# Kernel optimization log

Hardware: AMD Instinct MI355X
Metric: run time of the kernel (lower is better)

The kernel has to match this reference:

```python
import jax, jax.numpy as jnp
import numpy as np

L = 2048         # new tokens (prefill)
HID = 4096
NH = 32          # attention heads
NKV = 8          # kv heads
HD = HID // NH   # 128
MAX = 4096       # kv-cache capacity
EPS = 1e-5


def _rope_tables(L, HD):
    inv_freq = 1.0 / (10000.0 ** (np.arange(0, HD, 2, dtype=np.float32) / HD))
    ang = np.arange(L, dtype=np.float32)[:, None] * inv_freq[None, :]  # [L, HD/2]
    ang = np.concatenate([ang, ang], axis=-1)                          # HF duplicated layout
    return jnp.asarray(np.cos(ang)), jnp.asarray(np.sin(ang))


def setup_inputs() -> dict:
    key = jax.random.key(0)
    ks = jax.random.split(key, 6)
    cos, sin = _rope_tables(L, HD)
    s = 0.02
    return {
        "x": jax.random.normal(ks[0], (L, HID), jnp.float32),
        "cos": cos,
        "sin": sin,
        "position_ids": jnp.arange(L, dtype=jnp.int64),
        "seq_len": L,
        "k_cache": jnp.zeros((MAX, NKV, HD), jnp.float32),
        "v_cache": jnp.zeros((MAX, NKV, HD), jnp.float32),
        "ln_w": jnp.ones((HID,), jnp.float32),
        "Wq": jax.random.normal(ks[1], (NH * HD, HID), jnp.float32) * s,
        "Wk": jax.random.normal(ks[2], (NKV * HD, HID), jnp.float32) * s,
        "Wv": jax.random.normal(ks[3], (NKV * HD, HID), jnp.float32) * s,
        "Wo": jax.random.normal(ks[4], (HID, NH * HD), jnp.float32) * s,
    }


def _rms_norm(x, w, eps=EPS):
    xf = x.astype(jnp.float32)
    var = jnp.mean(xf * xf, axis=-1, keepdims=True)
    return (w * (xf * jax.lax.rsqrt(var + eps))).astype(x.dtype)


def _rotate_half(x):
    x1, x2 = jnp.split(x, 2, axis=-1)
    return jnp.concatenate([-x2, x1], axis=-1)


def reference(x, cos, sin, position_ids, seq_len, k_cache, v_cache, ln_w, Wq, Wk, Wv, Wo):
    Lq, hid = x.shape
    nkv, hd = k_cache.shape[1], k_cache.shape[2]
    nh = Wq.shape[0] // hd
    g = nh // nkv

    residual = x
    h = _rms_norm(x, ln_w)

    q = (h @ Wq.T).reshape(Lq, nh, hd)
    k = (h @ Wk.T).reshape(Lq, nkv, hd)
    v = (h @ Wv.T).reshape(Lq, nkv, hd)

    # RoPE, cos/sin broadcast over heads (unsqueeze_dim=1)
    c = cos[:, None, :]
    s = sin[:, None, :]
    q = q * c + _rotate_half(q) * s
    k = k * c + _rotate_half(k) * s

    # KV-cache scatter write
    k_cache = k_cache.at[position_ids].set(k)
    v_cache = v_cache.at[position_ids].set(v)

    # prefill path (num_new_tokens > 1): causal GQA SDPA over new keys only
    scale = 1.0 / jnp.sqrt(jnp.asarray(hd, jnp.float32))
    qg = q.reshape(Lq, nkv, g, hd)
    scores = jnp.einsum('qhgd,khd->hgqk', qg, k) * scale  # [nkv, g, Lq, Lq]
    idx = jnp.arange(Lq)
    causal = idx[None, :] <= idx[:, None]                  # [Lq, Lq]
    scores = jnp.where(causal[None, None], scores, -jnp.inf)
    p = jax.nn.softmax(scores, axis=-1)
    attn = jnp.einsum('hgqk,khd->qhgd', p, v).reshape(Lq, nh * hd)

    out = residual + attn @ Wo.T
    return out, k_cache, v_cache
```

## Files before the change

### kernel.cpp

```cpp
#include <hip/hip_runtime.h>
#include <hip/hip_bf16.h>
#include <cstdint>

#define L_SEQ 2048
#define HID   4096
#define NH    32
#define NKV   8
#define HD    128
#define MAXP  4096
#define QKVD  6144
#define K_OFF 4096
#define V_OFF 5120

using bf16_t = __hip_bfloat16;
typedef __bf16 bf16x8 __attribute__((ext_vector_type(8)));
typedef float  f32x4  __attribute__((ext_vector_type(4)));
typedef short  short4v __attribute__((ext_vector_type(4)));
typedef short  short8v __attribute__((ext_vector_type(8)));

__device__ __forceinline__ void async_copy16(void* lds, const void* g) {
  __builtin_amdgcn_global_load_lds(
      (__attribute__((address_space(1))) void*)g,
      (__attribute__((address_space(3))) void*)lds, 16, 0, 0);
}

__device__ __forceinline__ f32x4 MFMA16(bf16x8 a, bf16x8 b, f32x4 c) {
  return __builtin_amdgcn_mfma_f32_16x16x32_bf16(a, b, c, 0, 0, 0);
}

__global__ __launch_bounds__(256) void rmsnorm_kernel(
    const float* __restrict__ x, const float* __restrict__ w,
    bf16_t* __restrict__ h) {
  int row = blockIdx.x, t = threadIdx.x;
  const float4* xv = (const float4*)(x + (size_t)row * HID);
  float4 v[4];
  float ss = 0.f;
#pragma unroll
  for (int i = 0; i < 4; i++) {
    v[i] = xv[i * 256 + t];
    ss += v[i].x * v[i].x + v[i].y * v[i].y + v[i].z * v[i].z + v[i].w * v[i].w;
  }
#pragma unroll
  for (int off = 32; off >= 1; off >>= 1) ss += __shfl_xor(ss, off, 64);
  __shared__ float red[4];
  if ((t & 63) == 0) red[t >> 6] = ss;
  __syncthreads();
  float rr = rsqrtf((red[0] + red[1] + red[2] + red[3]) * (1.0f / HID) + 1e-5f);
  const float4* wv = (const float4*)w;
  bf16_t* hr = h + (size_t)row * HID;
#pragma unroll
  for (int i = 0; i < 4; i++) {
    float4 wl = wv[i * 256 + t];
    bf16_t tmp[4];
    tmp[0] = __float2bfloat16(v[i].x * rr * wl.x);
    tmp[1] = __float2bfloat16(v[i].y * rr * wl.y);
    tmp[2] = __float2bfloat16(v[i].z * rr * wl.z);
    tmp[3] = __float2bfloat16(v[i].w * rr * wl.w);
    *(short4v*)(hr + (size_t)(i * 256 + t) * 4) = *(short4v*)tmp;
  }
}

__global__ __launch_bounds__(256) void cvt_bf16_kernel(
    const float* __restrict__ src, bf16_t* __restrict__ dst) {
  size_t i = ((size_t)blockIdx.x * 256 + threadIdx.x) * 8;
  float4 a = *(const float4*)(src + i);
  float4 b = *(const float4*)(src + i + 4);
  bf16_t tmp[8] = {__float2bfloat16(a.x), __float2bfloat16(a.y),
                   __float2bfloat16(a.z), __float2bfloat16(a.w),
                   __float2bfloat16(b.x), __float2bfloat16(b.y),
                   __float2bfloat16(b.z), __float2bfloat16(b.w)};
  *(short8v*)(dst + i) = *(short8v*)tmp;
}

#define STR2_(x) #x
#define STR_(x) STR2_(x)

template <int OUT_MODE>
__global__ __launch_bounds__(512, 2) void gemm256_kernel(
    const bf16_t* __restrict__ A, const bf16_t* __restrict__ B,
    bf16_t* __restrict__ Cb, float* __restrict__ Cf,
    const float* __restrict__ resid, int N, int K) {
  __shared__ alignas(16) bf16_t As[2 * 2 * 8192];
  __shared__ alignas(16) bf16_t Bs[2 * 2 * 8192];

  const int t = threadIdx.x;
  const int l = t & 63;
  const int w = t >> 6;
  const int wm = w >> 2;
  const int wn = w & 3;
  const int wh = wn >> 1;
  const int wn1 = wn & 1;
  const int lane15 = l & 15, quad = l >> 4;
  const int l7 = l & 7;

  const bf16_t* Ag = A + (size_t)blockIdx.y * 256 * K;
  const bf16_t* Bg = B + (size_t)blockIdx.x * 256 * K;

  const int srow = t >> 3;
  const int sgran = (t & 7) ^ (srow & 7);
  const int wbase = w << 9;

  const bf16_t* pAg = Ag + (size_t)srow * K + sgran * 8;
  const bf16_t* pBg = Bg + (size_t)srow * K + sgran * 8;
  const size_t row64 = (size_t)64 * K;

#define STAGE(PL, UOFF, ldsh) do {                                            \
    const bf16_t* _g = (PL) + (UOFF);                                         \
    async_copy16((ldsh) + wbase, _g);                                         \
    async_copy16((ldsh) + wbase + 4096, _g + row64);                          \
  } while (0)

#define ASD(sl, h) (&As[(sl) * 16384 + (h) * 8192])
#define BSD(sl, h) (&Bs[(sl) * 16384 + (h) * 8192])

  typedef __attribute__((address_space(3))) char* lds_b;
  lds_b asb = (lds_b)As;
  lds_b bsb = (lds_b)Bs;
  const unsigned aoff0 = (unsigned)(wm * 16384 + lane15 * 128 + ((quad ^ l7) << 4));
  const unsigned boff0 = (unsigned)(wh * 16384 + (wn1 * 64 + lane15) * 128 + ((quad ^ l7) << 4));
  lds_b pa0s0 = asb + aoff0;
  lds_b pa1s0 = asb + (aoff0 ^ 64u);
  lds_b pa0s1 = pa0s0 + 32768;
  lds_b pa1s1 = pa1s0 + 32768;
  lds_b pb0s0 = bsb + boff0;
  lds_b pb1s0 = bsb + (boff0 ^ 64u);
  lds_b pb0s1 = pb0s0 + 32768;
  lds_b pb1s1 = pb1s0 + 32768;

#define DSR(dst, p, IMM) \
  asm volatile("ds_read_b128 %0, %1 offset:" STR_(IMM) : "=v"(dst) : "v"(p))

#define RA(dst, P0, P1, I0, I1, I2, I3) do {                                  \
    DSR(dst[0][0], P0, I0); DSR(dst[0][1], P1, I0);                           \
    DSR(dst[1][0], P0, I1); DSR(dst[1][1], P1, I1);                           \
    DSR(dst[2][0], P0, I2); DSR(dst[2][1], P1, I2);                           \
    DSR(dst[3][0], P0, I3); DSR(dst[3][1], P1, I3); } while (0)
#define RB(dst, P0, P1, I0, I1) do {                                          \
    DSR(dst[0][0], P0, I0); DSR(dst[0][1], P1, I0);                           \
    DSR(dst[1][0], P0, I1); DSR(dst[1][1], P1, I1); } while (0)

#define BAR() do { asm volatile("s_barrier");                                 \
    __builtin_amdgcn_sched_barrier(0); } while (0)
#define LGKM(NW) do { asm volatile("s_waitcnt lgkmcnt(" STR_(NW) ")");        \
    __builtin_amdgcn_sched_barrier(0); } while (0)
#define VMW(NW) asm volatile("s_waitcnt vmcnt(" STR_(NW) ")")

#define MMQ(IB, JB, AF, BF) do {                                              \
    __builtin_amdgcn_s_setprio(1);                                            \
    _Pragma("unroll") for (int i = 0; i < 4; i++)                             \
    _Pragma("unroll") for (int j = 0; j < 2; j++) {                           \
      acc[(IB)+i][(JB)+j] = MFMA16(AF[i][0], BF[j][0], acc[(IB)+i][(JB)+j]);  \
      acc[(IB)+i][(JB)+j] = MFMA16(AF[i][1], BF[j][1], acc[(IB)+i][(JB)+j]);  \
    }                                                                         \
    __builtin_amdgcn_s_setprio(0);                                            \
    __builtin_amdgcn_sched_barrier(0);                                        \
  } while (0)

  const size_t u128 = (size_t)128 * K;
  const int NTT = K >> 6;
  const int niter = NTT >> 1;

  f32x4 acc[8][4] = {};
  bf16x8 a[4][2], a2[4][2], blo[2][2], bhi[2][2];

  STAGE(pBg, 0,          BSD(0, 0));
  STAGE(pAg, 0,          ASD(0, 0));
  STAGE(pBg, u128,       BSD(0, 1));
  STAGE(pAg, u128,       ASD(0, 1));
  STAGE(pBg, 64,         BSD(1, 0));
  STAGE(pAg, 64,         ASD(1, 0));
  VMW(4);
  BAR();
  RA(a, pa0s0, pa1s0, 0, 2048, 4096, 6144);
  RB(blo, pb0s0, pb1s0, 0, 2048);

  for (int it = 0; it < niter; ++it) {
    const int tb = it * 2;
    const size_t kc1 = (size_t)((tb + 1) << 6);
    const size_t kc2 = (size_t)(((tb + 2 < NTT) ? tb + 2 : NTT - 1) << 6);
    const size_t kc3 = (size_t)(((tb + 3 < NTT) ? tb + 3 : NTT - 1) << 6);
    STAGE(pBg, u128 + kc1, BSD(1, 1));
    BAR();
    RB(bhi, pb0s0, pb1s0, 4096, 6144);
    LGKM(4);
    MMQ(0, 0, a, blo);
    BAR();
    STAGE(pAg, u128 + kc1, ASD(1, 1));
    BAR();
    RA(a2, pa0s0, pa1s0, 8192, 10240, 12288, 14336);
    LGKM(8);
    MMQ(0, 2, a, bhi);
    BAR();
    STAGE(pBg, kc2, BSD(0, 0));
    BAR();
    LGKM(0);
    MMQ(4, 0, a2, blo);
    BAR();
    STAGE(pAg, kc2, ASD(0, 0));
    VMW(4);
    BAR();
    RA(a, pa0s1, pa1s1, 0, 2048, 4096, 6144);
    RB(blo, pb0s1, pb1s1, 0, 2048);
    LGKM(12);
    MMQ(4, 2, a2, bhi);
    BAR();
    STAGE(pBg, u128 + kc2, BSD(0, 1));
    BAR();
    RB(bhi, pb0s1, pb1s1, 4096, 6144);
    LGKM(4);
    MMQ(0, 0, a, blo);
    BAR();
    STAGE(pAg, u128 + kc2, ASD(0, 1));
    BAR();
    RA(a2, pa0s1, pa1s1, 8192, 10240, 12288, 14336);
    LGKM(8);
    MMQ(0, 2, a, bhi);
    BAR();
    STAGE(pBg, kc3, BSD(1, 0));
    BAR();
    LGKM(0);
    MMQ(4, 0, a2, blo);
    BAR();
    STAGE(pAg, kc3, ASD(1, 0));
    VMW(4);
    BAR();
    if (it + 1 < niter) {
      RA(a, pa0s0, pa1s0, 0, 2048, 4096, 6144);
      RB(blo, pb0s0, pb1s0, 0, 2048);
    }
    LGKM(12);
    MMQ(4, 2, a2, bhi);
    BAR();
  }
  VMW(0);

  const int row0 = blockIdx.y * 256 + wm * 128 + quad * 4;
  const int col0 = blockIdx.x * 256 + wn * 64 + lane15;
#pragma unroll
  for (int i = 0; i < 8; i++)
#pragma unroll
    for (int j = 0; j < 4; j++)
#pragma unroll
      for (int r = 0; r < 4; r++) {
        size_t idx = (size_t)(row0 + i * 16 + r) * N + col0 + j * 16;
        if (OUT_MODE == 0)
          Cb[idx] = __float2bfloat16(acc[i][j][r]);
        else
          Cf[idx] = acc[i][j][r] + resid[idx];
      }
#undef STAGE
#undef ASD
#undef BSD
#undef DSR
#undef RA
#undef RB
#undef BAR
#undef LGKM
#undef VMW
#undef MMQ
}

__global__ __launch_bounds__(256) void rope_kernel(
    bf16_t* __restrict__ qkv,
    const float* __restrict__ cosT, const float* __restrict__ sinT,
    float* __restrict__ kc_out) {
  int idx = blockIdx.x * 256 + threadIdx.x;
  int d = idx & 63;
  int rest = idx >> 6;
  int hh = rest % (NH + NKV);
  int pos = rest / (NH + NKV);
  float c = cosT[pos * HD + d];
  float s = sinT[pos * HD + d];
  bf16_t* b = (hh < NH)
      ? qkv + (size_t)pos * QKVD + hh * HD
      : qkv + (size_t)pos * QKVD + K_OFF + (hh - NH) * HD;
  float x1 = __bfloat162float(b[d]);
  float x2 = __bfloat162float(b[d + 64]);
  float o1 = x1 * c - x2 * s;
  float o2 = x2 * c + x1 * s;
  b[d] = __float2bfloat16(o1);
  b[d + 64] = __float2bfloat16(o2);
  if (hh >= NH) {
    float* kc = kc_out + (size_t)pos * (NKV * HD) + (hh - NH) * HD;
    kc[d] = o1;
    kc[d + 64] = o2;
  }
}

__global__ __launch_bounds__(256) void vtrans_kernel(
    const bf16_t* __restrict__ qkv, float* __restrict__ vc_out,
    bf16_t* __restrict__ vT) {
  __shared__ alignas(16) short Ts[64 * 64];
  int kvh = blockIdx.x, pb = blockIdx.y, db = blockIdx.z;
  int t = threadIdx.x;
  int r = t & 63;
  int c4 = t >> 6;
  const short* src = (const short*)(qkv + (size_t)(pb * 64 + r) * QKVD +
                                    V_OFF + kvh * HD + db * 64 + c4 * 16);
  short8v v0 = *(const short8v*)src;
  short8v v1 = *(const short8v*)(src + 8);
  float* vo = vc_out + (size_t)(pb * 64 + r) * (NKV * HD) + kvh * HD + db * 64 + c4 * 16;
  float tmpf[16];
#pragma unroll
  for (int j = 0; j < 8; j++) {
    tmpf[j]     = __uint_as_float(((unsigned)(unsigned short)v0[j]) << 16);
    tmpf[j + 8] = __uint_as_float(((unsigned)(unsigned short)v1[j]) << 16);
  }
#pragma unroll
  for (int j = 0; j < 4; j++)
    ((float4*)vo)[j] = make_float4(tmpf[j * 4], tmpf[j * 4 + 1],
                                   tmpf[j * 4 + 2], tmpf[j * 4 + 3]);
  int cs = c4 ^ (r & 3);
  *(short8v*)&Ts[r * 64 + cs * 16] = v0;
  *(short8v*)&Ts[r * 64 + cs * 16 + 8] = v1;
  __syncthreads();
  int dr = t & 63;
  int pc = t >> 6;
  short vals[16];
#pragma unroll
  for (int j = 0; j < 16; j++) {
    int pos = pc * 16 + j;
    int cc = (dr >> 4) ^ (pos & 3);
    vals[j] = Ts[pos * 64 + cc * 16 + (dr & 15)];
  }
  short* dst = (short*)(vT + ((size_t)kvh * HD + db * 64 + dr) * L_SEQ + pb * 64 + pc * 16);
  *(short8v*)dst = *(short8v*)&vals[0];
  *(short8v*)(dst + 8) = *(short8v*)&vals[8];
}

__global__ __launch_bounds__(256) void cache_tail_kernel(
    const float* __restrict__ kc_in, const float* __restrict__ vc_in,
    float* __restrict__ kc_out, float* __restrict__ vc_out) {
  size_t base = (size_t)L_SEQ * NKV * HD;
  size_t i = base + ((size_t)blockIdx.x * 256 + threadIdx.x) * 4;
  *(float4*)(kc_out + i) = *(const float4*)(kc_in + i);
  *(float4*)(vc_out + i) = *(const float4*)(vc_in + i);
}

__global__ __launch_bounds__(256, 2) void attn_kernel(
    const bf16_t* __restrict__ qkv, const bf16_t* __restrict__ vT,
    bf16_t* __restrict__ attn) {
  int h = blockIdx.x;
  int pb = blockIdx.y;
  int kvh = h >> 2;
  int t = threadIdx.x, w = t >> 6, l = t & 63;
  int lane15 = l & 15, quad = l >> 4;

  __shared__ alignas(16) bf16_t Ks[2][16 * 512];
  __shared__ alignas(16) bf16_t Vs[2][16 * 512];
  __shared__ alignas(16) bf16_t Ps[4][16 * 68];

  const float scale = 0.08838834764831845f;

#define STAGEATTN(KB, BUF) do {                                               \
    _Pragma("unroll") for (int kk_ = 0; kk_ < 4; kk_++)                       \
      async_copy16(&Ks[BUF][(w * 4 + kk_) * 512],                             \
                   qkv + (size_t)((KB) * 64 + w * 16 + lane15) * QKVD +       \
                       K_OFF + kvh * HD + kk_ * 32 + quad * 8);               \
    _Pragma("unroll") for (int j_ = 0; j_ < 4; j_++) {                        \
      int tt_ = w * 2 + (j_ >> 1), kt_ = j_ & 1;                              \
      async_copy16(&Vs[BUF][(tt_ * 2 + kt_) * 512],                           \
                   vT + ((size_t)kvh * HD + tt_ * 16 + lane15) * L_SEQ +      \
                       (KB) * 64 + kt_ * 32 + quad * 8);                      \
    }                                                                         \
  } while (0)

  for (int sel = 0; sel < 2; ++sel) {
    const int qb = sel ? 31 - pb : pb;

    bf16x8 aq[4];
#pragma unroll
    for (int kk = 0; kk < 4; kk++)
      aq[kk] = *(const bf16x8*)(qkv +
          (size_t)(qb * 64 + w * 16 + lane15) * QKVD +
          h * HD + kk * 32 + quad * 8);

    f32x4 o[8] = {};
    float lsum[4] = {};
    const int nk = qb + 1;

    STAGEATTN(0, 0);
    for (int kblk = 0; kblk < nk; kblk++) {
      const int cur = kblk & 1;
      if (kblk + 1 < nk) {
        STAGEATTN(kblk + 1, cur ^ 1);
        asm volatile("s_waitcnt vmcnt(8)");
      } else {
        asm volatile("s_waitcnt vmcnt(0)");
      }
      __builtin_amdgcn_s_barrier();
      __builtin_amdgcn_sched_barrier(0);

      f32x4 sacc[4] = {};
      __builtin_amdgcn_s_setprio(1);
#pragma unroll
      for (int n = 0; n < 4; n++)
#pragma unroll
        for (int kk = 0; kk < 4; kk++) {
          bf16x8 b = *(const bf16x8*)&Ks[cur][(n * 4 + kk) * 512 + l * 8];
          sacc[n] = MFMA16(aq[kk], b, sacc[n]);
        }
      __builtin_amdgcn_s_setprio(0);

      bool maskblk = (kblk == qb);
#pragma unroll
      for (int n = 0; n < 4; n++) {
        int col = kblk * 64 + n * 16 + lane15;
#pragma unroll
        for (int r = 0; r < 4; r++) {
          float p = __expf(sacc[n][r] * scale);
          if (maskblk && col > (qb * 64 + w * 16 + quad * 4 + r)) p = 0.f;
          lsum[r] += p;
          Ps[w][(quad * 4 + r) * 68 + n * 16 + lane15] = __float2bfloat16(p);
        }
      }

      __builtin_amdgcn_s_setprio(1);
#pragma unroll
      for (int kt2 = 0; kt2 < 2; kt2++) {
        bf16x8 ap = *(const bf16x8*)&Ps[w][lane15 * 68 + kt2 * 32 + quad * 8];
#pragma unroll
        for (int tt = 0; tt < 8; tt++) {
          bf16x8 b = *(const bf16x8*)&Vs[cur][(tt * 2 + kt2) * 512 + l * 8];
          o[tt] = MFMA16(ap, b, o[tt]);
        }
      }
      __builtin_amdgcn_s_setprio(0);
      __builtin_amdgcn_s_barrier();
    }

    float inv[4];
#pragma unroll
    for (int r = 0; r < 4; r++) {
      float s = lsum[r];
#pragma unroll
      for (int off = 1; off < 16; off <<= 1) s += __shfl_xor(s, off, 64);
      inv[r] = 1.f / s;
    }
    int qrow0 = qb * 64 + w * 16;
#pragma unroll
    for (int tt = 0; tt < 8; tt++) {
      int col = h * HD + tt * 16 + lane15;
#pragma unroll
      for (int r = 0; r < 4; r++)
        attn[(size_t)(qrow0 + quad * 4 + r) * HID + col] =
            __float2bfloat16(o[tt][r] * inv[r]);
    }
  }
#undef STAGEATTN
}

extern "C" void kernel_launch(void* const* d_in, const int* in_sizes, int n_in,
                              void* d_out, int out_size, void* d_ws, size_t ws_size,
                              hipStream_t stream) {
  const float* x    = (const float*)d_in[0];
  const float* cosT = (const float*)d_in[1];
  const float* sinT = (const float*)d_in[2];
  const float* kc_in = (const float*)d_in[5];
  const float* vc_in = (const float*)d_in[6];
  const float* ln_w  = (const float*)d_in[7];
  const float* Wq = (const float*)d_in[8];
  const float* Wk = (const float*)d_in[9];
  const float* Wv = (const float*)d_in[10];
  const float* Wo = (const float*)d_in[11];

  float* out    = (float*)d_out;
  float* kc_out = out + (size_t)L_SEQ * HID;
  float* vc_out = kc_out + (size_t)MAXP * NKV * HD;

  char* ws = (char*)d_ws;
  bf16_t* h_bf    = (bf16_t*)(ws + 0);
  bf16_t* attn_bf = (bf16_t*)(ws + 0);
  bf16_t* Wqkv_bf = (bf16_t*)(ws + 16777216);
  bf16_t* Wo_bf   = (bf16_t*)(ws + 16777216);
  bf16_t* qkv_bf  = (bf16_t*)(ws + 67108864);
  bf16_t* vT_bf   = (bf16_t*)(ws + 92274688);

  rmsnorm_kernel<<<L_SEQ, 256, 0, stream>>>(x, ln_w, h_bf);
  cvt_bf16_kernel<<<(HID * HID) / (8 * 256), 256, 0, stream>>>(Wq, Wqkv_bf);
  cvt_bf16_kernel<<<(NKV * HD * HID) / (8 * 256), 256, 0, stream>>>(
      Wk, Wqkv_bf + (size_t)K_OFF * HID);
  cvt_bf16_kernel<<<(NKV * HD * HID) / (8 * 256), 256, 0, stream>>>(
      Wv, Wqkv_bf + (size_t)V_OFF * HID);

  gemm256_kernel<0><<<dim3(QKVD / 256, L_SEQ / 256), 512, 0, stream>>>(
      h_bf, Wqkv_bf, qkv_bf, nullptr, nullptr, QKVD, HID);

  rope_kernel<<<(L_SEQ * (NH + NKV) * 64) / 256, 256, 0, stream>>>(
      qkv_bf, cosT, sinT, kc_out);
  vtrans_kernel<<<dim3(NKV, L_SEQ / 64, HD / 64), 256, 0, stream>>>(
      qkv_bf, vc_out, vT_bf);
  cache_tail_kernel<<<((MAXP - L_SEQ) * NKV * HD) / (4 * 256), 256, 0, stream>>>(
      kc_in, vc_in, kc_out, vc_out);

  cvt_bf16_kernel<<<(HID * HID) / (8 * 256), 256, 0, stream>>>(Wo, Wo_bf);

  attn_kernel<<<dim3(NH, 16), 256, 0, stream>>>(qkv_bf, vT_bf, attn_bf);

  gemm256_kernel<1><<<dim3(HID / 256, L_SEQ / 256), 512, 0, stream>>>(
      attn_bf, Wo_bf, nullptr, out, x, HID, HID);
}
```

Measured before the change: 542.7 us.

## Split-K the output projection GEMM and fuse QKV weight conversions

```diff
diff --git a/kernel.cpp b/kernel.cpp
--- a/kernel.cpp
+++ b/kernel.cpp
@@ -72,6 +72,34 @@
   *(short8v*)(dst + i) = *(short8v*)tmp;
 }
 
+__global__ __launch_bounds__(256) void cvtqkv_kernel(
+    const float* __restrict__ Wq, const float* __restrict__ Wk,
+    const float* __restrict__ Wv, bf16_t* __restrict__ dst) {
+  size_t i = ((size_t)blockIdx.x * 256 + threadIdx.x) * 8;
+  size_t row = i >> 12;
+  const float* src;
+  size_t off;
+  if (row < 4096)      { src = Wq; off = i; }
+  else if (row < 5120) { src = Wk; off = i - ((size_t)4096 << 12); }
+  else                 { src = Wv; off = i - ((size_t)5120 << 12); }
+  float4 a = *(const float4*)(src + off);
+  float4 b = *(const float4*)(src + off + 4);
+  bf16_t tmp[8] = {__float2bfloat16(a.x), __float2bfloat16(a.y),
+                   __float2bfloat16(a.z), __float2bfloat16(a.w),
+                   __float2bfloat16(b.x), __float2bfloat16(b.y),
+                   __float2bfloat16(b.z), __float2bfloat16(b.w)};
+  *(short8v*)(dst + i) = *(short8v*)tmp;
+}
+
+__global__ __launch_bounds__(256) void addp_kernel(
+    float* __restrict__ out, const float* __restrict__ P) {
+  size_t i = ((size_t)blockIdx.x * 256 + threadIdx.x) * 4;
+  float4 o = *(float4*)(out + i);
+  float4 p = *(const float4*)(P + i);
+  o.x += p.x; o.y += p.y; o.z += p.z; o.w += p.w;
+  *(float4*)(out + i) = o;
+}
+
 #define STR2_(x) #x
 #define STR_(x) STR2_(x)
 
@@ -79,7 +107,8 @@
 __global__ __launch_bounds__(512, 2) void gemm256_kernel(
     const bf16_t* __restrict__ A, const bf16_t* __restrict__ B,
     bf16_t* __restrict__ Cb, float* __restrict__ Cf,
-    const float* __restrict__ resid, int N, int K) {
+    const float* __restrict__ resid, float* __restrict__ Pout,
+    int N, int K, int LDA) {
   __shared__ alignas(16) bf16_t As[2 * 2 * 8192];
   __shared__ alignas(16) bf16_t Bs[2 * 2 * 8192];
 
@@ -93,16 +122,17 @@
   const int lane15 = l & 15, quad = l >> 4;
   const int l7 = l & 7;
 
-  const bf16_t* Ag = A + (size_t)blockIdx.y * 256 * K;
-  const bf16_t* Bg = B + (size_t)blockIdx.x * 256 * K;
+  const size_t koff = (size_t)blockIdx.z * K;
+  const bf16_t* Ag = A + (size_t)blockIdx.y * 256 * LDA + koff;
+  const bf16_t* Bg = B + (size_t)blockIdx.x * 256 * LDA + koff;
 
   const int srow = t >> 3;
   const int sgran = (t & 7) ^ (srow & 7);
   const int wbase = w << 9;
 
-  const bf16_t* pAg = Ag + (size_t)srow * K + sgran * 8;
-  const bf16_t* pBg = Bg + (size_t)srow * K + sgran * 8;
-  const size_t row64 = (size_t)64 * K;
+  const bf16_t* pAg = Ag + (size_t)srow * LDA + sgran * 8;
+  const bf16_t* pBg = Bg + (size_t)srow * LDA + sgran * 8;
+  const size_t row64 = (size_t)64 * LDA;
 
 #define STAGE(PL, UOFF, ldsh) do {                                            \
     const bf16_t* _g = (PL) + (UOFF);                                         \
@@ -156,7 +186,7 @@
     __builtin_amdgcn_sched_barrier(0);                                        \
   } while (0)
 
-  const size_t u128 = (size_t)128 * K;
+  const size_t u128 = (size_t)128 * LDA;
   const int NTT = K >> 6;
   const int niter = NTT >> 1;
 
@@ -243,10 +273,14 @@
 #pragma unroll
       for (int r = 0; r < 4; r++) {
         size_t idx = (size_t)(row0 + i * 16 + r) * N + col0 + j * 16;
-        if (OUT_MODE == 0)
+        if (OUT_MODE == 0) {
           Cb[idx] = __float2bfloat16(acc[i][j][r]);
-        else
-          Cf[idx] = acc[i][j][r] + resid[idx];
+        } else {
+          if (blockIdx.z == 0)
+            Cf[idx] = acc[i][j][r] + resid[idx];
+          else
+            Pout[idx] = acc[i][j][r];
+        }
       }
 #undef STAGE
 #undef ASD
@@ -473,18 +507,16 @@
   bf16_t* attn_bf = (bf16_t*)(ws + 0);
   bf16_t* Wqkv_bf = (bf16_t*)(ws + 16777216);
   bf16_t* Wo_bf   = (bf16_t*)(ws + 16777216);
+  float*  Psplit  = (float*)(ws + 50331648);
   bf16_t* qkv_bf  = (bf16_t*)(ws + 67108864);
   bf16_t* vT_bf   = (bf16_t*)(ws + 92274688);
 
   rmsnorm_kernel<<<L_SEQ, 256, 0, stream>>>(x, ln_w, h_bf);
-  cvt_bf16_kernel<<<(HID * HID) / (8 * 256), 256, 0, stream>>>(Wq, Wqkv_bf);
-  cvt_bf16_kernel<<<(NKV * HD * HID) / (8 * 256), 256, 0, stream>>>(
-      Wk, Wqkv_bf + (size_t)K_OFF * HID);
-  cvt_bf16_kernel<<<(NKV * HD * HID) / (8 * 256), 256, 0, stream>>>(
-      Wv, Wqkv_bf + (size_t)V_OFF * HID);
-
-  gemm256_kernel<0><<<dim3(QKVD / 256, L_SEQ / 256), 512, 0, stream>>>(
-      h_bf, Wqkv_bf, qkv_bf, nullptr, nullptr, QKVD, HID);
+  cvtqkv_kernel<<<(QKVD * HID) / (8 * 256), 256, 0, stream>>>(
+      Wq, Wk, Wv, Wqkv_bf);
+
+  gemm256_kernel<0><<<dim3(QKVD / 256, L_SEQ / 256, 1), 512, 0, stream>>>(
+      h_bf, Wqkv_bf, qkv_bf, nullptr, nullptr, nullptr, QKVD, HID, HID);
 
   rope_kernel<<<(L_SEQ * (NH + NKV) * 64) / 256, 256, 0, stream>>>(
       qkv_bf, cosT, sinT, kc_out);
@@ -497,6 +529,7 @@
 
   attn_kernel<<<dim3(NH, 16), 256, 0, stream>>>(qkv_bf, vT_bf, attn_bf);
 
-  gemm256_kernel<1><<<dim3(HID / 256, L_SEQ / 256), 512, 0, stream>>>(
-      attn_bf, Wo_bf, nullptr, out, x, HID, HID);
-}
+  gemm256_kernel<3><<<dim3(HID / 256, L_SEQ / 256, 2), 512, 0, stream>>>(
+      attn_bf, Wo_bf, nullptr, out, x, Psplit, HID, HID / 2, HID);
+  addp_kernel<<<(L_SEQ * HID) / (4 * 256), 256, 0, stream>>>(out, Psplit);
+}
```

Measured after the change: 568.2 us. 4.7% more time.
